# Kernel tuning notes

Measured on AMD Instinct MI355X. Metric: run time of the kernel, lower is better.

## Reference

```python
import jax, jax.numpy as jnp
import numpy as np

B, I, H = 8192, 1024, 1024

def setup_inputs() -> dict:
    key = jax.random.key(0)
    ks = jax.random.split(key, 6)
    s_in = 1.0 / np.sqrt(I)
    s_h = 1.0 / np.sqrt(H)
    return {
        "x": jax.random.normal(ks[0], (B, I), jnp.float32),
        "h_prev": jax.random.normal(ks[1], (B, H), jnp.float32),
        "c_prev": jax.random.normal(ks[2], (B, H), jnp.float32),
        "Wx": jax.random.normal(ks[3], (4, H, I), jnp.float32) * s_in,   # gate order: input, forget, cell, output
        "Wh": jax.random.normal(ks[4], (4, H, H), jnp.float32) * s_h,
        "bh": jax.random.normal(ks[5], (4, H), jnp.float32) * s_h,
    }

def reference(x, h_prev, c_prev, Wx, Wh, bh):
    # Fused: 2 batched GEMMs for all 4 gates -> [B, 4, H]
    gates = (jnp.einsum('bi,ghi->bgh', x, Wx)
             + jnp.einsum('bk,ghk->bgh', h_prev, Wh)
             + bh[None, :, :])
    i = jax.nn.sigmoid(gates[:, 0])
    f = jax.nn.sigmoid(gates[:, 1])
    g = jnp.tanh(gates[:, 2])
    o = jax.nn.sigmoid(gates[:, 3])
    c_next = f * c_prev + i * g
    h_next = o * jnp.tanh(c_next)
    return (h_next, c_next)
```

## Files before the change

kernel.cpp:

```cpp
#include <hip/hip_runtime.h>
#include <hip/hip_bf16.h>
#include <stdint.h>

#define B_DIM 8192
#define I_DIM 1024
#define H_DIM 1024

typedef __attribute__((ext_vector_type(8))) short short8;
typedef __attribute__((ext_vector_type(4))) float f32x4;

static __device__ __forceinline__ short f2b(float f) {
    __bf16 h = (__bf16)f;
    return __builtin_bit_cast(short, h);
}

static __device__ __forceinline__ short8 pack8(float4 a, float4 b) {
    short8 s;
    s[0] = f2b(a.x); s[1] = f2b(a.y); s[2] = f2b(a.z); s[3] = f2b(a.w);
    s[4] = f2b(b.x); s[5] = f2b(b.y); s[6] = f2b(b.z); s[7] = f2b(b.w);
    return s;
}

static __device__ __forceinline__ float sigmoid_f(float x) {
    return 1.0f / (1.0f + __expf(-x));
}

static __device__ __forceinline__ float tanh_fast(float x) {
    x = fminf(fmaxf(x, -15.0f), 15.0f);
    float e = __expf(2.0f * x);
    return (e - 1.0f) / (e + 1.0f);
}

static __device__ __forceinline__ void load_lds16(const void* gptr, void* lptr) {
    __builtin_amdgcn_global_load_lds(
        (const __attribute__((address_space(1))) uint32_t*)gptr,
        (__attribute__((address_space(3))) uint32_t*)lptr, 16, 0, 0);
}

#define GA_GROUPS (512 * 32 * 2 * 64)
#define GB_GROUPS (256 * 32 * 2 * 64)

__global__ __launch_bounds__(256) void convert_kernel(
    const float* __restrict__ x, const float* __restrict__ h,
    const float* __restrict__ wx, const float* __restrict__ wh,
    short* __restrict__ Aw, short* __restrict__ Bw)
{
    const int64_t total = (int64_t)GA_GROUPS + GB_GROUPS;
    for (int64_t g = (int64_t)blockIdx.x * blockDim.x + threadIdx.x; g < total;
         g += (int64_t)gridDim.x * blockDim.x) {
        const float* src;
        short* dst;
        if (g < GA_GROUPS) {
            const int lane = (int)(g & 63);
            const int rest = (int)(g >> 6);
            const int kh   = rest & 1;
            const int tk   = (rest >> 1) & 31;
            const int mfrag = rest >> 6;
            const int row = (mfrag << 4) + (lane & 15);
            const int k   = (tk << 6) + (kh << 5) + ((lane >> 4) << 3);
            src = (k < 1024) ? (x + (size_t)row * 1024 + k)
                             : (h + (size_t)row * 1024 + (k - 1024));
            dst = Aw + (size_t)g * 8;
        } else {
            const int64_t gb = g - GA_GROUPS;
            const int lane = (int)(gb & 63);
            const int rest = (int)(gb >> 6);
            const int kh   = rest & 1;
            const int tk   = (rest >> 1) & 31;
            const int nfrag = rest >> 6;
            const int cf   = nfrag & 15;
            const int bn   = nfrag >> 4;
            const int gate = cf & 3;
            const int col  = (bn << 6) + ((cf >> 2) << 4) + (lane & 15);
            const int k    = (tk << 6) + (kh << 5) + ((lane >> 4) << 3);
            src = (k < 1024) ? (wx + ((size_t)(gate << 10) + col) * 1024 + k)
                             : (wh + ((size_t)(gate << 10) + col) * 1024 + (k - 1024));
            dst = Bw + (size_t)gb * 8;
        }
        float4 v0 = ((const float4*)src)[0];
        float4 v1 = ((const float4*)src)[1];
        *(short8*)dst = pack8(v0, v1);
    }
}

__global__ __launch_bounds__(512, 4) void lstm_gemm_tlp_kernel(
    const short* __restrict__ Aw, const short* __restrict__ Bw,
    const float* __restrict__ cprev, const float* __restrict__ bh,
    float* __restrict__ out)
{
    __shared__ __align__(16) short smem[24576];

    const int bid = blockIdx.x;
    const int xcd = bid & 7;
    const int c   = bid >> 3;
    const int bm  = c >> 1;
    const int bn  = 2 * xcd + (c & 1);
    const int m0  = bm * 128;
    const int h0  = bn * 64;

    const int t    = threadIdx.x;
    const int lane = t & 63;
    const int w    = t >> 6;
    const int wm   = w >> 2;
    const int wn   = w & 3;
    const int lc   = lane & 15;

    const short* aSrc  = Aw + (size_t)(bm * 8  + w)         * 32768 + lane * 8;
    const short* bSrc0 = Bw + (size_t)(bn * 16 + 2 * w)     * 32768 + lane * 8;
    const short* bSrc1 = Bw + (size_t)(bn * 16 + 2 * w + 1) * 32768 + lane * 8;

    f32x4 acc[4][4] = {};

    load_lds16(aSrc,  &smem[w * 512]);
    load_lds16(bSrc0, &smem[4096 + (2 * w) * 512]);
    load_lds16(bSrc1, &smem[4096 + (2 * w + 1) * 512]);
    asm volatile("s_waitcnt vmcnt(0)" ::: "memory");
    __builtin_amdgcn_s_barrier();

    #pragma unroll 1
    for (int tk = 0; tk < 64; ++tk) {
        const int d  = (tk & 1) * 12288;
        const int dn = 12288 - d;
        const int tp = (tk + 1 < 64) ? tk + 1 : tk;

        short8 bv[4], av[4];
        #pragma unroll
        for (int j = 0; j < 4; ++j)
            bv[j] = *(const short8*)&smem[d + 4096 + (wn * 4 + j) * 512 + lane * 8];
        #pragma unroll
        for (int i = 0; i < 4; ++i)
            av[i] = *(const short8*)&smem[d + (wm * 4 + i) * 512 + lane * 8];

        load_lds16(aSrc  + tp * 512, &smem[dn + w * 512]);
        load_lds16(bSrc0 + tp * 512, &smem[dn + 4096 + (2 * w) * 512]);
        load_lds16(bSrc1 + tp * 512, &smem[dn + 4096 + (2 * w + 1) * 512]);

        __builtin_amdgcn_s_setprio(1);
        #pragma unroll
        for (int i = 0; i < 4; ++i)
            #pragma unroll
            for (int j = 0; j < 4; ++j)
                acc[i][j] = __builtin_amdgcn_mfma_f32_16x16x32_bf16(
                    av[i], bv[j], acc[i][j], 0, 0, 0);
        __builtin_amdgcn_s_setprio(0);

        asm volatile("s_waitcnt vmcnt(0)" ::: "memory");
        __builtin_amdgcn_s_barrier();
    }

    const int rg = lane >> 4;
    const int h  = h0 + wn * 16 + lc;
    const float b_i = bh[0 * H_DIM + h];
    const float b_f = bh[1 * H_DIM + h];
    const float b_g = bh[2 * H_DIM + h];
    const float b_o = bh[3 * H_DIM + h];

    #pragma unroll
    for (int mf = 0; mf < 4; ++mf) {
        #pragma unroll
        for (int r = 0; r < 4; ++r) {
            const int row = m0 + wm * 64 + mf * 16 + rg * 4 + r;
            const float pi = acc[mf][0][r] + b_i;
            const float pf = acc[mf][1][r] + b_f;
            const float pg = acc[mf][2][r] + b_g;
            const float po = acc[mf][3][r] + b_o;
            const float iv = sigmoid_f(pi);
            const float fv = sigmoid_f(pf);
            const float gv = tanh_fast(pg);
            const float ov = sigmoid_f(po);
            const float cp = cprev[(size_t)row * H_DIM + h];
            const float cn = fv * cp + iv * gv;
            const float hn = ov * tanh_fast(cn);
            out[(size_t)row * H_DIM + h] = hn;
            out[(size_t)B_DIM * H_DIM + (size_t)row * H_DIM + h] = cn;
        }
    }
}

static __device__ __forceinline__ int swz(int row, int k) {
    int byte = (row << 7) + (k << 1);
    byte ^= (row & 7) << 4;
    return byte >> 1;
}

__global__ __launch_bounds__(256, 2) void lstm_fallback_kernel(
    const float* __restrict__ x, const float* __restrict__ hprev,
    const float* __restrict__ cprev, const float* __restrict__ Wx,
    const float* __restrict__ Wh, const float* __restrict__ bh,
    float* __restrict__ out)
{
    __shared__ __align__(16) short As[128 * 64];
    __shared__ __align__(16) short Bs[128 * 64];

    int bid = blockIdx.x;
    bid = (bid & 7) * 256 + (bid >> 3);
    const int mt = bid >> 5;
    const int ht = bid & 31;
    const int m0 = mt * 128;
    const int h0 = ht * 32;

    const int t    = threadIdx.x;
    const int lane = t & 63;
    const int w    = t >> 6;
    const int wr   = w >> 1;
    const int wc   = w & 1;

    const int srow = t >> 3;
    const int sk   = (t & 7) * 8;

    f32x4 acc[4][4] = {};

    #pragma unroll 1
    for (int phase = 0; phase < 2; ++phase) {
        const float* __restrict__ Ap = phase ? hprev : x;
        const float* __restrict__ Bp = phase ? Wh : Wx;
        #pragma unroll 1
        for (int kk = 0; kk < 1024; kk += 64) {
            __syncthreads();
            #pragma unroll
            for (int p = 0; p < 4; ++p) {
                const int row = srow + p * 32;
                const float4* src = (const float4*)(Ap + (size_t)(m0 + row) * I_DIM + kk + sk);
                *(short8*)&As[swz(row, sk)] = pack8(src[0], src[1]);
            }
            #pragma unroll
            for (int p = 0; p < 4; ++p) {
                const int n    = srow + p * 32;
                const int gate = (n >> 4) & 3;
                const int hcol = h0 + ((n >> 6) << 4) + (n & 15);
                const float4* src = (const float4*)(Bp + (size_t)((gate << 10) + hcol) * 1024 + kk + sk);
                *(short8*)&Bs[swz(n, sk)] = pack8(src[0], src[1]);
            }
            __syncthreads();
            #pragma unroll
            for (int ks = 0; ks < 2; ++ks) {
                const int kb = ks * 32 + ((lane >> 4) << 3);
                short8 a[4], b[4];
                #pragma unroll
                for (int m = 0; m < 4; ++m)
                    a[m] = *(const short8*)&As[swz(wr * 64 + m * 16 + (lane & 15), kb)];
                #pragma unroll
                for (int j = 0; j < 4; ++j)
                    b[j] = *(const short8*)&Bs[swz(wc * 64 + j * 16 + (lane & 15), kb)];
                #pragma unroll
                for (int m = 0; m < 4; ++m)
                    #pragma unroll
                    for (int j = 0; j < 4; ++j)
                        acc[m][j] = __builtin_amdgcn_mfma_f32_16x16x32_bf16(a[m], b[j], acc[m][j], 0, 0, 0);
            }
        }
    }

    const int cl = lane & 15;
    const int rg = lane >> 4;
    const int h  = h0 + wc * 16 + cl;
    const float b_i = bh[0 * H_DIM + h];
    const float b_f = bh[1 * H_DIM + h];
    const float b_g = bh[2 * H_DIM + h];
    const float b_o = bh[3 * H_DIM + h];

    #pragma unroll
    for (int m = 0; m < 4; ++m) {
        #pragma unroll
        for (int r = 0; r < 4; ++r) {
            const int row = m0 + wr * 64 + m * 16 + rg * 4 + r;
            const float pi = acc[m][0][r] + b_i;
            const float pf = acc[m][1][r] + b_f;
            const float pg = acc[m][2][r] + b_g;
            const float po = acc[m][3][r] + b_o;
            const float iv = sigmoid_f(pi);
            const float fv = sigmoid_f(pf);
            const float gv = tanh_fast(pg);
            const float ov = sigmoid_f(po);
            const float cp = cprev[(size_t)row * H_DIM + h];
            const float cn = fv * cp + iv * gv;
            const float hn = ov * tanh_fast(cn);
            out[(size_t)row * H_DIM + h] = hn;
            out[(size_t)B_DIM * H_DIM + (size_t)row * H_DIM + h] = cn;
        }
    }
}

extern "C" void kernel_launch(void* const* d_in, const int* in_sizes, int n_in,
                              void* d_out, int out_size, void* d_ws, size_t ws_size,
                              hipStream_t stream) {
    const float* x     = (const float*)d_in[0];
    const float* hprev = (const float*)d_in[1];
    const float* cprev = (const float*)d_in[2];
    const float* Wx    = (const float*)d_in[3];
    const float* Wh    = (const float*)d_in[4];
    const float* bh    = (const float*)d_in[5];
    float* out = (float*)d_out;

    const size_t need = ((size_t)B_DIM * 2048 + (size_t)4096 * 2048) * sizeof(short);
    if (ws_size >= need && d_ws != nullptr) {
        short* Aw = (short*)d_ws;
        short* Bw = Aw + (size_t)512 * 32768;
        hipLaunchKernelGGL(convert_kernel, dim3(4096), dim3(256), 0, stream,
                           x, hprev, Wx, Wh, Aw, Bw);
        hipLaunchKernelGGL(lstm_gemm_tlp_kernel, dim3(1024), dim3(512), 0, stream,
                           Aw, Bw, cprev, bh, out);
    } else {
        hipLaunchKernelGGL(lstm_fallback_kernel, dim3(2048), dim3(256), 0, stream,
                           x, hprev, cprev, Wx, Wh, bh, out);
    }
}
```

Before: 149.1 us.

## Shrink GEMM block tile to 128x128 with 4 waves and unroll double-buffer loop

The fused LSTM GEMM block changes from 512 threads computing 128 rows by 64 hidden units (256 gate columns) to 256 threads computing 128 rows by 32 hidden units (128 gate columns). The grid doubles to 2048 blocks and LDS per block drops. The K loop is unrolled by two so the double-buffer offsets become compile-time constants. This trades less B-tile reuse per block and more global/L2 traffic for A for smaller blocks and more of them resident per CU, and each wave now issues four async loads per step instead of three.

```diff
diff --git a/kernel.cpp b/kernel.cpp
--- a/kernel.cpp
+++ b/kernel.cpp
@@ -83,73 +83,79 @@
     }
 }
 
-__global__ __launch_bounds__(512, 4) void lstm_gemm_tlp_kernel(
+#define AOFF(d, f) ((d) * 8192 + (f) * 512)
+#define BOFF(d, f) ((d) * 8192 + 4096 + (f) * 512)
+
+__global__ __launch_bounds__(256, 4) void lstm_gemm_tlp_kernel(
     const short* __restrict__ Aw, const short* __restrict__ Bw,
     const float* __restrict__ cprev, const float* __restrict__ bh,
     float* __restrict__ out)
 {
-    __shared__ __align__(16) short smem[24576];
+    __shared__ __align__(16) short smem[16384];
 
     const int bid = blockIdx.x;
     const int xcd = bid & 7;
     const int c   = bid >> 3;
-    const int bm  = c >> 1;
-    const int bn  = 2 * xcd + (c & 1);
+    const int bm  = c >> 2;
+    const int ht  = 4 * xcd + (c & 3);
     const int m0  = bm * 128;
-    const int h0  = bn * 64;
 
     const int t    = threadIdx.x;
     const int lane = t & 63;
     const int w    = t >> 6;
-    const int wm   = w >> 2;
-    const int wn   = w & 3;
+    const int wm   = w >> 1;
+    const int wn   = w & 1;
     const int lc   = lane & 15;
 
-    const short* aSrc  = Aw + (size_t)(bm * 8  + w)         * 32768 + lane * 8;
-    const short* bSrc0 = Bw + (size_t)(bn * 16 + 2 * w)     * 32768 + lane * 8;
-    const short* bSrc1 = Bw + (size_t)(bn * 16 + 2 * w + 1) * 32768 + lane * 8;
+    const short* aSrc0 = Aw + (size_t)(bm * 8 + 2 * w)     * 32768 + lane * 8;
+    const short* aSrc1 = Aw + (size_t)(bm * 8 + 2 * w + 1) * 32768 + lane * 8;
+    const short* bSrc0 = Bw + (size_t)(ht * 8 + 2 * w)     * 32768 + lane * 8;
+    const short* bSrc1 = Bw + (size_t)(ht * 8 + 2 * w + 1) * 32768 + lane * 8;
 
     f32x4 acc[4][4] = {};
 
-    load_lds16(aSrc,  &smem[w * 512]);
-    load_lds16(bSrc0, &smem[4096 + (2 * w) * 512]);
-    load_lds16(bSrc1, &smem[4096 + (2 * w + 1) * 512]);
+    load_lds16(aSrc0, &smem[AOFF(0, 2 * w)]);
+    load_lds16(aSrc1, &smem[AOFF(0, 2 * w + 1)]);
+    load_lds16(bSrc0, &smem[BOFF(0, 2 * w)]);
+    load_lds16(bSrc1, &smem[BOFF(0, 2 * w + 1)]);
     asm volatile("s_waitcnt vmcnt(0)" ::: "memory");
     __builtin_amdgcn_s_barrier();
 
+#define TILE(d, tp) do { \
+    short8 bv[4], av[4]; \
+    _Pragma("unroll") \
+    for (int j = 0; j < 4; ++j) \
+        bv[j] = *(const short8*)&smem[BOFF(d, wn * 4 + j) + lane * 8]; \
+    _Pragma("unroll") \
+    for (int i = 0; i < 4; ++i) \
+        av[i] = *(const short8*)&smem[AOFF(d, wm * 4 + i) + lane * 8]; \
+    load_lds16(aSrc0 + (tp) * 512, &smem[AOFF(d ^ 1, 2 * w)]); \
+    load_lds16(aSrc1 + (tp) * 512, &smem[AOFF(d ^ 1, 2 * w + 1)]); \
+    load_lds16(bSrc0 + (tp) * 512, &smem[BOFF(d ^ 1, 2 * w)]); \
+    load_lds16(bSrc1 + (tp) * 512, &smem[BOFF(d ^ 1, 2 * w + 1)]); \
+    __builtin_amdgcn_s_setprio(1); \
+    _Pragma("unroll") \
+    for (int i = 0; i < 4; ++i) \
+        _Pragma("unroll") \
+        for (int j = 0; j < 4; ++j) \
+            acc[i][j] = __builtin_amdgcn_mfma_f32_16x16x32_bf16( \
+                av[i], bv[j], acc[i][j], 0, 0, 0); \
+    __builtin_amdgcn_s_setprio(0); \
+    asm volatile("s_waitcnt vmcnt(0)" ::: "memory"); \
+    __builtin_amdgcn_s_barrier(); \
+} while (0)
+
     #pragma unroll 1
-    for (int tk = 0; tk < 64; ++tk) {
-        const int d  = (tk & 1) * 12288;
-        const int dn = 12288 - d;
-        const int tp = (tk + 1 < 64) ? tk + 1 : tk;
-
-        short8 bv[4], av[4];
-        #pragma unroll
-        for (int j = 0; j < 4; ++j)
-            bv[j] = *(const short8*)&smem[d + 4096 + (wn * 4 + j) * 512 + lane * 8];
-        #pragma unroll
-        for (int i = 0; i < 4; ++i)
-            av[i] = *(const short8*)&smem[d + (wm * 4 + i) * 512 + lane * 8];
-
-        load_lds16(aSrc  + tp * 512, &smem[dn + w * 512]);
-        load_lds16(bSrc0 + tp * 512, &smem[dn + 4096 + (2 * w) * 512]);
-        load_lds16(bSrc1 + tp * 512, &smem[dn + 4096 + (2 * w + 1) * 512]);
-
-        __builtin_amdgcn_s_setprio(1);
-        #pragma unroll
-        for (int i = 0; i < 4; ++i)
-            #pragma unroll
-            for (int j = 0; j < 4; ++j)
-                acc[i][j] = __builtin_amdgcn_mfma_f32_16x16x32_bf16(
-                    av[i], bv[j], acc[i][j], 0, 0, 0);
-        __builtin_amdgcn_s_setprio(0);
-
-        asm volatile("s_waitcnt vmcnt(0)" ::: "memory");
-        __builtin_amdgcn_s_barrier();
-    }
+    for (int tk2 = 0; tk2 < 32; ++tk2) {
+        const int t1 = 2 * tk2 + 1;
+        const int t2 = (t1 + 1 < 64) ? t1 + 1 : t1;
+        TILE(0, t1);
+        TILE(1, t2);
+    }
+#undef TILE
 
     const int rg = lane >> 4;
-    const int h  = h0 + wn * 16 + lc;
+    const int h  = ht * 32 + wn * 16 + lc;
     const float b_i = bh[0 * H_DIM + h];
     const float b_f = bh[1 * H_DIM + h];
     const float b_g = bh[2 * H_DIM + h];
@@ -298,7 +304,7 @@
         short* Bw = Aw + (size_t)512 * 32768;
         hipLaunchKernelGGL(convert_kernel, dim3(4096), dim3(256), 0, stream,
                            x, hprev, Wx, Wh, Aw, Bw);
-        hipLaunchKernelGGL(lstm_gemm_tlp_kernel, dim3(1024), dim3(512), 0, stream,
+        hipLaunchKernelGGL(lstm_gemm_tlp_kernel, dim3(2048), dim3(256), 0, stream,
                            Aw, Bw, cprev, bh, out);
     } else {
         hipLaunchKernelGGL(lstm_fallback_kernel, dim3(2048), dim3(256), 0, stream,
```

Measured after the change: 152.2 us. 2.1% more time.
